# Performance work log

Measured on AMD Instinct MI355X. Metric: run time of the kernel, lower is better.

Reference implementation:

```python
import jax, jax.numpy as jnp
import numpy as np


def _lstm_scan(x_tbd, h0, c0, Wi, Wh, b):
    # x_tbd: [T, B, D]; standard LSTMCell, gate order i, f, g, o.
    def step(carry, xt):
        h, c = carry
        gates = xt @ Wi.T + h @ Wh.T + b  # [B, 4H]
        i, f, g, o = jnp.split(gates, 4, axis=-1)
        c = jax.nn.sigmoid(f) * c + jax.nn.sigmoid(i) * jnp.tanh(g)
        h = jax.nn.sigmoid(o) * jnp.tanh(c)
        return (h, c), h
    _, ys = jax.lax.scan(step, (h0, c0), x_tbd)
    return ys  # [T, B, H]


def setup_inputs() -> dict:
    key = jax.random.key(0)
    ks = jax.random.split(key, 8)
    B, T, D, H = 64, 512, 512, 512
    inputs_emb = jax.random.normal(ks[0], (B, T, D), dtype=jnp.float32)
    # variable sequence lengths in [T//2, T], mask = 1 for valid positions
    lengths = jax.random.randint(ks[1], (B,), T // 2, T + 1)
    mask = (jnp.arange(T)[None, :] < lengths[:, None]).astype(jnp.float32)
    s = 1.0 / np.sqrt(H)
    return {
        "inputs_emb": inputs_emb,
        "mask": mask,
        "h0": jnp.zeros((B, H), jnp.float32),
        "c0": jnp.zeros((B, H), jnp.float32),
        "Wi_f": jax.random.uniform(ks[2], (4 * H, D), jnp.float32, -s, s),
        "Wh_f": jax.random.uniform(ks[3], (4 * H, H), jnp.float32, -s, s),
        "b_f": jnp.zeros((4 * H,), jnp.float32),
        "Wi_b": jax.random.uniform(ks[4], (4 * H, D), jnp.float32, -s, s),
        "Wh_b": jax.random.uniform(ks[5], (4 * H, H), jnp.float32, -s, s),
        "b_b": jnp.zeros((4 * H,), jnp.float32),
    }


def reference(inputs_emb, mask, h0, c0, Wi_f, Wh_f, b_f, Wi_b, Wh_b, b_b):
    B, T, D = inputs_emb.shape
    # ---- forward direction ----
    ys_f = _lstm_scan(inputs_emb.transpose(1, 0, 2), h0, c0, Wi_f, Wh_f, b_f)  # [T,B,H]
    out_f = ys_f.transpose(1, 0, 2)  # [B,T,H]
    # ---- backward direction with gather-based reordering ----
    lengths = mask.astype(jnp.int32).sum(axis=1)  # [B]
    t_idx = jnp.arange(T)[None, :]
    # index_b: rotate so padding comes first: [len..T-1] ++ [0..len-1]
    idx_b = (t_idx + lengths[:, None]) % T  # [B,T]
    # index_f: rotate back: [T-len..T-1] ++ [0..T-len-1]
    idx_f = (t_idx + (T - lengths)[:, None]) % T  # [B,T]
    x_b = jnp.take_along_axis(inputs_emb, idx_b[:, :, None], axis=1)  # [B,T,D]
    # run cell over reversed time, then reverse collected outputs back
    x_b_rev = x_b.transpose(1, 0, 2)[::-1]  # [T,B,D], t = T-1 .. 0
    ys_b_rev = _lstm_scan(x_b_rev, h0, c0, Wi_b, Wh_b, b_b)  # [T,B,H]
    out_b = ys_b_rev[::-1].transpose(1, 0, 2)  # [B,T,H], time order
    out_b = jnp.take_along_axis(out_b, idx_f[:, :, None], axis=1)
    return jnp.concatenate([out_f, out_b], axis=-1)  # [B,T,2H]
```

## Files before the change

### kernel.cpp

```cpp
#include <hip/hip_runtime.h>
#include <hip/hip_fp16.h>

typedef _Float16 f16x8 __attribute__((ext_vector_type(8)));
typedef float f32x4 __attribute__((ext_vector_type(4)));

#define TT 512
#define HH 512
#define BB 64

#define WS_FLAGS 0
#define WS_LENS  4096
#define WS_HBUF  8192

#define LDS_W     0
#define LDS_GLDS  131072
#define LDS_H     135424
#define LDS_TOTAL 151808

#define MFMA(a, b, c) __builtin_amdgcn_mfma_f32_16x16x32_f16((a), (b), (c), 0, 0, 0)

__device__ __forceinline__ float fsig(float x) {
  float ax = __builtin_fabsf(x);
  float t  = __builtin_amdgcn_exp2f(-1.442695041f * ax);
  float r  = __builtin_amdgcn_rcpf(1.0f + t);
  return x >= 0.0f ? r : t * r;
}
__device__ __forceinline__ float ftanh_(float x) {
  float ax = __builtin_fabsf(x);
  float t  = __builtin_amdgcn_exp2f(-2.885390082f * ax);
  float r  = (1.0f - t) * __builtin_amdgcn_rcpf(1.0f + t);
  return x >= 0.0f ? r : -r;
}

__global__ void len_kernel(const float* __restrict__ mask, int* __restrict__ lens) {
  int b = threadIdx.x;
  if (b < BB) {
    float s = 0.f;
    for (int t = 0; t < TT; ++t) s += mask[b * TT + t];
    lens[b] = (int)(s + 0.5f);
  }
}

__global__ void __launch_bounds__(256, 1)
bilstm_kernel(const float* __restrict__ x, const int* __restrict__ lens,
              const float* __restrict__ h0, const float* __restrict__ c0,
              const float* __restrict__ Wi_f, const float* __restrict__ Wh_f,
              const float* __restrict__ b_f,
              const float* __restrict__ Wi_b, const float* __restrict__ Wh_b,
              const float* __restrict__ b_b,
              float* __restrict__ out, __half* hbuf, int* flags)
{
  extern __shared__ __align__(16) char smem[];
  f16x8* wlds = (f16x8*)(smem + LDS_W);
  float (*glds)[68] = (float (*)[68])(smem + LDS_GLDS);
  char* htile = smem + LDS_H;

  const int bid = blockIdx.x;
  const int dir = bid >> 7;
  const int bg  = (bid >> 5) & 3;
  const int cg  = bid & 31;
  const int tid = threadIdx.x;
  const int wv  = tid >> 6;
  const int ln  = tid & 63;
  const int il  = ln & 15;
  const int kg  = ln >> 4;

  const float* Wi = dir ? Wi_b : Wi_f;
  const float* Wh = dir ? Wh_b : Wh_f;
  const float* bv = dir ? b_b  : b_f;

  __half* hb = hbuf + (size_t)dir * (2 * BB * HH);
  int* fl = flags + (dir * 4 + bg) * 32;

  const int jrow = wv * HH + cg * 16 + il;
#pragma unroll 4
  for (int kk = 0; kk < 32; ++kk) {
    int k0 = kk * 32 + kg * 8;
    const float* src = (k0 < 512) ? (Wi + (size_t)jrow * 512 + k0)
                                  : (Wh + (size_t)jrow * 512 + (k0 - 512));
    float4 f0 = *(const float4*)(src);
    float4 f1 = *(const float4*)(src + 4);
    f16x8 w;
    w[0] = (_Float16)f0.x; w[1] = (_Float16)f0.y; w[2] = (_Float16)f0.z; w[3] = (_Float16)f0.w;
    w[4] = (_Float16)f1.x; w[5] = (_Float16)f1.y; w[6] = (_Float16)f1.z; w[7] = (_Float16)f1.w;
    wlds[(wv * 32 + kk) * 64 + ln] = w;
  }
  const f16x8* wbase = wlds + (size_t)wv * 32 * 64 + ln;

  const int bl_e  = tid >> 4;
  const int i_e   = tid & 15;
  const int b_e   = bg * 16 + bl_e;
  const int col_e = cg * 16 + i_e;
  float cst = c0[(size_t)b_e * HH + col_e];
  const float bi_ = bv[0 * HH + col_e];
  const float bf_ = bv[1 * HH + col_e];
  const float bg_ = bv[2 * HH + col_e];
  const float bo_ = bv[3 * HH + col_e];
  const int len_e = lens[b_e];

  const int b_g   = bg * 16 + il;
  const int len_b = lens[b_g];

  {
    unsigned short hbits = __half_as_ushort(__float2half(h0[(size_t)b_e * HH + col_e]));
    unsigned short* p = (unsigned short*)(hb + (size_t)1 * BB * HH + (size_t)b_e * HH + col_e);
    __hip_atomic_store(p, hbits, __ATOMIC_RELAXED, __HIP_MEMORY_SCOPE_AGENT);
  }
  __syncthreads();
  if (tid == 0)
    __hip_atomic_store(&fl[cg], 1, __ATOMIC_RELAXED, __HIP_MEMORY_SCOPE_AGENT);

  const int hrbase = tid >> 7;
  const int hinrow = (tid & 127) * 8;

  for (int t = 0; t < TT; ++t) {
    int tsrc;
    if (dir == 0) tsrc = t;
    else { int v = len_b + (TT - 1) - t; if (v >= TT) v -= TT; tsrc = v; }
    const float* xrow = x + ((size_t)b_g * TT + tsrc) * 512;
    float4 xr[32];
#pragma unroll
    for (int q = 0; q < 32; ++q)
      xr[q] = *(const float4*)(xrow + (q >> 1) * 32 + kg * 8 + (q & 1) * 4);

    {
      const int need = t + 1;
      while (1) {
        int v = __hip_atomic_load(&fl[ln & 31], __ATOMIC_RELAXED, __HIP_MEMORY_SCOPE_AGENT);
        if (__all(v >= need)) break;
        __builtin_amdgcn_s_sleep(1);
      }
    }

    const unsigned long long* hsrc = (const unsigned long long*)
        (hb + (size_t)((t + 1) & 1) * BB * HH + (size_t)bg * 16 * HH);
    unsigned long long hv64[8];
#pragma unroll
    for (int s = 0; s < 8; ++s)
      hv64[s] = __hip_atomic_load(hsrc + s * 256 + tid, __ATOMIC_RELAXED, __HIP_MEMORY_SCOPE_AGENT);

    f16x8 ax[16];
#pragma unroll
    for (int kk = 0; kk < 16; ++kk) {
      float4 f0 = xr[kk * 2], f1 = xr[kk * 2 + 1];
      f16x8 w;
      w[0] = (_Float16)f0.x; w[1] = (_Float16)f0.y; w[2] = (_Float16)f0.z; w[3] = (_Float16)f0.w;
      w[4] = (_Float16)f1.x; w[5] = (_Float16)f1.y; w[6] = (_Float16)f1.z; w[7] = (_Float16)f1.w;
      ax[kk] = w;
    }

#pragma unroll
    for (int s = 0; s < 8; ++s) {
      int row = s * 2 + hrbase;
      *(unsigned long long*)(htile + row * 1024 + (hinrow ^ ((row & 7) << 4))) = hv64[s];
    }
    __syncthreads();

    f16x8 fh[16];
#pragma unroll
    for (int kk = 0; kk < 16; ++kk) {
      int inr = kk * 64 + kg * 16;
      fh[kk] = *(const f16x8*)(htile + il * 1024 + (inr ^ ((il & 7) << 4)));
    }

    f32x4 ac0 = {0.f,0.f,0.f,0.f}, ac1 = {0.f,0.f,0.f,0.f};
    f32x4 ac2 = {0.f,0.f,0.f,0.f}, ac3 = {0.f,0.f,0.f,0.f};
#pragma unroll
    for (int kk = 0; kk < 16; kk += 4) {
      ac0 = MFMA(ax[kk + 0], wbase[(kk + 0) * 64], ac0);
      ac1 = MFMA(ax[kk + 1], wbase[(kk + 1) * 64], ac1);
      ac2 = MFMA(ax[kk + 2], wbase[(kk + 2) * 64], ac2);
      ac3 = MFMA(ax[kk + 3], wbase[(kk + 3) * 64], ac3);
    }
#pragma unroll
    for (int kk = 0; kk < 16; kk += 4) {
      ac0 = MFMA(fh[kk + 0], wbase[(16 + kk + 0) * 64], ac0);
      ac1 = MFMA(fh[kk + 1], wbase[(16 + kk + 1) * 64], ac1);
      ac2 = MFMA(fh[kk + 2], wbase[(16 + kk + 2) * 64], ac2);
      ac3 = MFMA(fh[kk + 3], wbase[(16 + kk + 3) * 64], ac3);
    }

#pragma unroll
    for (int r = 0; r < 4; ++r)
      glds[kg * 4 + r][wv * 16 + il] = ac0[r] + ac1[r] + ac2[r] + ac3[r];
    __syncthreads();

    float gi = glds[bl_e][ 0 + i_e] + bi_;
    float gf = glds[bl_e][16 + i_e] + bf_;
    float gg = glds[bl_e][32 + i_e] + bg_;
    float go = glds[bl_e][48 + i_e] + bo_;
    float si = fsig(gi), sf = fsig(gf), so = fsig(go);
    float tg = ftanh_(gg);
    cst = sf * cst + si * tg;
    float hv = so * ftanh_(cst);

    unsigned short hbits = __half_as_ushort(__float2half(hv));
    unsigned short* hp = (unsigned short*)(hb + (size_t)(t & 1) * BB * HH + (size_t)b_e * HH + col_e);
    __hip_atomic_store(hp, hbits, __ATOMIC_RELAXED, __HIP_MEMORY_SCOPE_AGENT);

    __syncthreads();
    if (tid == 0)
      __hip_atomic_store(&fl[cg], t + 2, __ATOMIC_RELAXED, __HIP_MEMORY_SCOPE_AGENT);

    if (dir == 0) {
      out[((size_t)b_e * TT + t) * (2 * HH) + col_e] = hv;
    } else {
      int td = len_e - 1 - t; if (td < 0) td += TT;
      out[((size_t)b_e * TT + td) * (2 * HH) + HH + col_e] = hv;
    }
  }
}

extern "C" void kernel_launch(void* const* d_in, const int* in_sizes, int n_in,
                              void* d_out, int out_size, void* d_ws, size_t ws_size,
                              hipStream_t stream) {
  const float* x    = (const float*)d_in[0];
  const float* mask = (const float*)d_in[1];
  const float* h0   = (const float*)d_in[2];
  const float* c0   = (const float*)d_in[3];
  const float* Wi_f = (const float*)d_in[4];
  const float* Wh_f = (const float*)d_in[5];
  const float* b_f  = (const float*)d_in[6];
  const float* Wi_b = (const float*)d_in[7];
  const float* Wh_b = (const float*)d_in[8];
  const float* b_b  = (const float*)d_in[9];
  float* out = (float*)d_out;

  char* ws = (char*)d_ws;
  int*    flags = (int*)(ws + WS_FLAGS);
  int*    lens  = (int*)(ws + WS_LENS);
  __half* hbuf  = (__half*)(ws + WS_HBUF);

  hipMemsetAsync(ws, 0, 4096, stream);

  hipLaunchKernelGGL(len_kernel, dim3(1), dim3(64), 0, stream, mask, lens);

  hipFuncSetAttribute((const void*)bilstm_kernel,
                      hipFuncAttributeMaxDynamicSharedMemorySize, LDS_TOTAL);

  hipLaunchKernelGGL(bilstm_kernel, dim3(256), dim3(256), LDS_TOTAL, stream,
                     x, lens, h0, c0, Wi_f, Wh_f, b_f, Wi_b, Wh_b, b_b,
                     out, hbuf, flags);
}
```

Before: 2.800 ms.

## Replace per-block flag barrier with step-tagged hidden-state words and overlap x-GEMM

Removes the separate per-block progress flags and packs each fp16 hidden value together with a 16-bit timestep tag into a 32-bit word. Consumers speculatively load h, run the input-projection MFMAs, then re-poll only the chunks whose tags are stale. This drops one __syncthreads and the flag store/poll round trip per step, and overlaps the x·Wi work with waiting on the other blocks. The cost is doubled hidden-buffer traffic (32-bit words instead of 16-bit) plus a larger memset, and correctness now rests on per-word tag visibility under relaxed atomics.

```diff
diff --git a/kernel.cpp b/kernel.cpp
--- a/kernel.cpp
+++ b/kernel.cpp
@@ -8,9 +8,9 @@
 #define HH 512
 #define BB 64
 
-#define WS_FLAGS 0
 #define WS_LENS  4096
 #define WS_HBUF  8192
+#define WS_END   (8192 + 524288)
 
 #define LDS_W     0
 #define LDS_GLDS  131072
@@ -48,7 +48,7 @@
               const float* __restrict__ b_f,
               const float* __restrict__ Wi_b, const float* __restrict__ Wh_b,
               const float* __restrict__ b_b,
-              float* __restrict__ out, __half* hbuf, int* flags)
+              float* __restrict__ out, unsigned int* hbuf)
 {
   extern __shared__ __align__(16) char smem[];
   f16x8* wlds = (f16x8*)(smem + LDS_W);
@@ -69,8 +69,7 @@
   const float* Wh = dir ? Wh_b : Wh_f;
   const float* bv = dir ? b_b  : b_f;
 
-  __half* hb = hbuf + (size_t)dir * (2 * BB * HH);
-  int* fl = flags + (dir * 4 + bg) * 32;
+  unsigned int* hb32 = hbuf + (size_t)dir * (2 * BB * HH);
 
   const int jrow = wv * HH + cg * 16 + il;
 #pragma unroll 4
@@ -103,64 +102,38 @@
 
   {
     unsigned short hbits = __half_as_ushort(__float2half(h0[(size_t)b_e * HH + col_e]));
-    unsigned short* p = (unsigned short*)(hb + (size_t)1 * BB * HH + (size_t)b_e * HH + col_e);
-    __hip_atomic_store(p, hbits, __ATOMIC_RELAXED, __HIP_MEMORY_SCOPE_AGENT);
+    unsigned int w0 = (1u << 16) | (unsigned int)hbits;
+    __hip_atomic_store(hb32 + (size_t)1 * BB * HH + (size_t)b_e * HH + col_e, w0,
+                       __ATOMIC_RELAXED, __HIP_MEMORY_SCOPE_AGENT);
   }
   __syncthreads();
-  if (tid == 0)
-    __hip_atomic_store(&fl[cg], 1, __ATOMIC_RELAXED, __HIP_MEMORY_SCOPE_AGENT);
-
-  const int hrbase = tid >> 7;
-  const int hinrow = (tid & 127) * 8;
 
   for (int t = 0; t < TT; ++t) {
+    const unsigned int* hs = hb32 + (size_t)((t + 1) & 1) * BB * HH + (size_t)bg * 16 * HH;
+    const unsigned int expT = (unsigned int)(t + 1);
+    unsigned int hwv[8][4];
+#pragma unroll
+    for (int j = 0; j < 8; ++j) {
+      const unsigned int* p = hs + j * 1024 + tid * 4;
+      hwv[j][0] = __hip_atomic_load(p + 0, __ATOMIC_RELAXED, __HIP_MEMORY_SCOPE_AGENT);
+      hwv[j][1] = __hip_atomic_load(p + 1, __ATOMIC_RELAXED, __HIP_MEMORY_SCOPE_AGENT);
+      hwv[j][2] = __hip_atomic_load(p + 2, __ATOMIC_RELAXED, __HIP_MEMORY_SCOPE_AGENT);
+      hwv[j][3] = __hip_atomic_load(p + 3, __ATOMIC_RELAXED, __HIP_MEMORY_SCOPE_AGENT);
+    }
+
     int tsrc;
     if (dir == 0) tsrc = t;
     else { int v = len_b + (TT - 1) - t; if (v >= TT) v -= TT; tsrc = v; }
     const float* xrow = x + ((size_t)b_g * TT + tsrc) * 512;
-    float4 xr[32];
-#pragma unroll
-    for (int q = 0; q < 32; ++q)
-      xr[q] = *(const float4*)(xrow + (q >> 1) * 32 + kg * 8 + (q & 1) * 4);
-
-    {
-      const int need = t + 1;
-      while (1) {
-        int v = __hip_atomic_load(&fl[ln & 31], __ATOMIC_RELAXED, __HIP_MEMORY_SCOPE_AGENT);
-        if (__all(v >= need)) break;
-        __builtin_amdgcn_s_sleep(1);
-      }
-    }
-
-    const unsigned long long* hsrc = (const unsigned long long*)
-        (hb + (size_t)((t + 1) & 1) * BB * HH + (size_t)bg * 16 * HH);
-    unsigned long long hv64[8];
-#pragma unroll
-    for (int s = 0; s < 8; ++s)
-      hv64[s] = __hip_atomic_load(hsrc + s * 256 + tid, __ATOMIC_RELAXED, __HIP_MEMORY_SCOPE_AGENT);
-
     f16x8 ax[16];
 #pragma unroll
     for (int kk = 0; kk < 16; ++kk) {
-      float4 f0 = xr[kk * 2], f1 = xr[kk * 2 + 1];
+      float4 f0 = *(const float4*)(xrow + kk * 32 + kg * 8);
+      float4 f1 = *(const float4*)(xrow + kk * 32 + kg * 8 + 4);
       f16x8 w;
       w[0] = (_Float16)f0.x; w[1] = (_Float16)f0.y; w[2] = (_Float16)f0.z; w[3] = (_Float16)f0.w;
       w[4] = (_Float16)f1.x; w[5] = (_Float16)f1.y; w[6] = (_Float16)f1.z; w[7] = (_Float16)f1.w;
       ax[kk] = w;
-    }
-
-#pragma unroll
-    for (int s = 0; s < 8; ++s) {
-      int row = s * 2 + hrbase;
-      *(unsigned long long*)(htile + row * 1024 + (hinrow ^ ((row & 7) << 4))) = hv64[s];
-    }
-    __syncthreads();
-
-    f16x8 fh[16];
-#pragma unroll
-    for (int kk = 0; kk < 16; ++kk) {
-      int inr = kk * 64 + kg * 16;
-      fh[kk] = *(const f16x8*)(htile + il * 1024 + (inr ^ ((il & 7) << 4)));
     }
 
     f32x4 ac0 = {0.f,0.f,0.f,0.f}, ac1 = {0.f,0.f,0.f,0.f};
@@ -172,6 +145,51 @@
       ac2 = MFMA(ax[kk + 2], wbase[(kk + 2) * 64], ac2);
       ac3 = MFMA(ax[kk + 3], wbase[(kk + 3) * 64], ac3);
     }
+
+    unsigned int pend = 0;
+#pragma unroll
+    for (int j = 0; j < 8; ++j) {
+      bool ok = ((hwv[j][0] >> 16) == expT) && ((hwv[j][1] >> 16) == expT) &&
+                ((hwv[j][2] >> 16) == expT) && ((hwv[j][3] >> 16) == expT);
+      if (!ok) pend |= (1u << j);
+    }
+    while (pend) {
+      __builtin_amdgcn_s_sleep(2);
+#pragma unroll
+      for (int j = 0; j < 8; ++j) {
+        if (pend & (1u << j)) {
+          const unsigned int* p = hs + j * 1024 + tid * 4;
+          unsigned int a0 = __hip_atomic_load(p + 0, __ATOMIC_RELAXED, __HIP_MEMORY_SCOPE_AGENT);
+          unsigned int a1 = __hip_atomic_load(p + 1, __ATOMIC_RELAXED, __HIP_MEMORY_SCOPE_AGENT);
+          unsigned int a2 = __hip_atomic_load(p + 2, __ATOMIC_RELAXED, __HIP_MEMORY_SCOPE_AGENT);
+          unsigned int a3 = __hip_atomic_load(p + 3, __ATOMIC_RELAXED, __HIP_MEMORY_SCOPE_AGENT);
+          if (((a0 >> 16) == expT) && ((a1 >> 16) == expT) &&
+              ((a2 >> 16) == expT) && ((a3 >> 16) == expT)) {
+            hwv[j][0] = a0; hwv[j][1] = a1; hwv[j][2] = a2; hwv[j][3] = a3;
+            pend &= ~(1u << j);
+          }
+        }
+      }
+    }
+
+#pragma unroll
+    for (int j = 0; j < 8; ++j) {
+      int row = j * 2 + (tid >> 7);
+      unsigned int lo = (hwv[j][0] & 0xFFFFu) | (hwv[j][1] << 16);
+      unsigned int hi = (hwv[j][2] & 0xFFFFu) | (hwv[j][3] << 16);
+      int byo = (((tid & 127) * 8) ^ ((row & 7) << 4));
+      uint2 v; v.x = lo; v.y = hi;
+      *(uint2*)(htile + row * 1024 + byo) = v;
+    }
+    __syncthreads();
+
+    f16x8 fh[16];
+#pragma unroll
+    for (int kk = 0; kk < 16; ++kk) {
+      int inr = kk * 64 + kg * 16;
+      fh[kk] = *(const f16x8*)(htile + il * 1024 + (inr ^ ((il & 7) << 4)));
+    }
+
 #pragma unroll
     for (int kk = 0; kk < 16; kk += 4) {
       ac0 = MFMA(fh[kk + 0], wbase[(16 + kk + 0) * 64], ac0);
@@ -194,13 +212,12 @@
     cst = sf * cst + si * tg;
     float hv = so * ftanh_(cst);
 
-    unsigned short hbits = __half_as_ushort(__float2half(hv));
-    unsigned short* hp = (unsigned short*)(hb + (size_t)(t & 1) * BB * HH + (size_t)b_e * HH + col_e);
-    __hip_atomic_store(hp, hbits, __ATOMIC_RELAXED, __HIP_MEMORY_SCOPE_AGENT);
-
-    __syncthreads();
-    if (tid == 0)
-      __hip_atomic_store(&fl[cg], t + 2, __ATOMIC_RELAXED, __HIP_MEMORY_SCOPE_AGENT);
+    {
+      unsigned short hbits = __half_as_ushort(__float2half(hv));
+      unsigned int pw = ((unsigned int)(t + 2) << 16) | (unsigned int)hbits;
+      __hip_atomic_store(hb32 + (size_t)(t & 1) * BB * HH + (size_t)b_e * HH + col_e, pw,
+                         __ATOMIC_RELAXED, __HIP_MEMORY_SCOPE_AGENT);
+    }
 
     if (dir == 0) {
       out[((size_t)b_e * TT + t) * (2 * HH) + col_e] = hv;
@@ -227,11 +244,10 @@
   float* out = (float*)d_out;
 
   char* ws = (char*)d_ws;
-  int*    flags = (int*)(ws + WS_FLAGS);
-  int*    lens  = (int*)(ws + WS_LENS);
-  __half* hbuf  = (__half*)(ws + WS_HBUF);
-
-  hipMemsetAsync(ws, 0, 4096, stream);
+  int*          lens = (int*)(ws + WS_LENS);
+  unsigned int* hbuf = (unsigned int*)(ws + WS_HBUF);
+
+  hipMemsetAsync(ws, 0, WS_END, stream);
 
   hipLaunchKernelGGL(len_kernel, dim3(1), dim3(64), 0, stream, mask, lens);
 
@@ -240,5 +256,5 @@
 
   hipLaunchKernelGGL(bilstm_kernel, dim3(256), dim3(256), LDS_TOTAL, stream,
                      x, lens, h0, c0, Wi_f, Wh_f, b_f, Wi_b, Wh_b, b_b,
-                     out, hbuf, flags);
-}
+                     out, hbuf);
+}
```

Result: slower. 5.161 ms (+84.3%).
